# Kernel tuning notes

Measured on AMD Instinct MI355X. Metric: run time of the kernel, lower is better.

## Reference

```python
import jax, jax.numpy as jnp
import numpy as np
from jax import lax

B, C, IC, H, W = 4, 64, 32, 64, 64


def _conv(x, w, b, stride, pad):
    y = lax.conv_general_dilated(
        x, w, (stride, stride), [(pad, pad), (pad, pad)],
        dimension_numbers=('NCHW', 'OIHW', 'NCHW'))
    return y + b[None, :, None, None]


def setup_inputs() -> dict:
    key = jax.random.key(0)
    ks = jax.random.split(key, 15)
    s = 0.05
    inp = {
        'x': jax.random.normal(ks[0], (B, C, H, W), jnp.float32),
        # GEunit convs (3x3)
        'd1_w': jax.random.normal(ks[1], (C, C, 3, 3), jnp.float32) * s,
        'd1_b': jax.random.normal(ks[2], (C,), jnp.float32) * s,
        'd2_w': jax.random.normal(ks[3], (C, C, 3, 3), jnp.float32) * s,
        'd2_b': jax.random.normal(ks[4], (C,), jnp.float32) * s,
        'd3_w': jax.random.normal(ks[5], (C, C, 3, 3), jnp.float32) * s,
        'd3_b': jax.random.normal(ks[6], (C,), jnp.float32) * s,
        # 1x1 projections
        'g_w': jax.random.normal(ks[7], (IC, C, 1, 1), jnp.float32) * s,
        'g_b': jax.random.normal(ks[8], (IC,), jnp.float32) * s,
        'th_w': jax.random.normal(ks[9], (IC, C, 1, 1), jnp.float32) * s,
        'th_b': jax.random.normal(ks[10], (IC,), jnp.float32) * s,
        'ph_w': jax.random.normal(ks[11], (IC, C, 1, 1), jnp.float32) * s,
        'ph_b': jax.random.normal(ks[12], (IC,), jnp.float32) * s,
        # output projection (zero-init in original; random here for nontrivial baseline)
        'w_w': jax.random.normal(ks[13], (C, IC, 1, 1), jnp.float32) * s,
        'w_b': jax.random.normal(ks[14], (C,), jnp.float32) * s,
    }
    return inp


def _forward(x, d1_w, d1_b, d2_w, d2_b, d3_w, d3_b,
             g_w, g_b, th_w, th_b, ph_w, ph_b, w_w, w_b):
    lrelu = lambda v: jnp.where(v >= 0, v, 0.2 * v)
    y = lrelu(_conv(x, d1_w, d1_b, 2, 1))
    y = lrelu(_conv(y, d2_w, d2_b, 2, 1))
    y = _conv(y, d3_w, d3_b, 2, 1)
    y = jax.image.resize(y, (x.shape[0], x.shape[1], x.shape[2], x.shape[3]),
                         method='bilinear')  # align_corners=False equivalent
    am = jax.nn.sigmoid(y) * x  # attention_map, [B,C,H,W]

    b, c, h, w = am.shape
    n = h * w
    g_x = _conv(am, g_w, g_b, 1, 0).reshape(b, IC, n)      # [B,IC,N]
    theta = _conv(am, th_w, th_b, 1, 0).reshape(b, IC, n)  # [B,IC,N]
    phi = _conv(am, ph_w, ph_b, 1, 0).reshape(b, IC, n)    # [B,IC,N]

    # f[b,i,j] = theta[:, i] . phi[:, j];  softmax over dim=1 (the i axis)
    f = jnp.einsum('bci,bcj->bij', theta, phi)             # [B,N,N]
    f_div_C = jax.nn.softmax(f, axis=1)
    y2 = jnp.einsum('bij,bjc->bic', f_div_C, g_x.transpose(0, 2, 1))  # [B,N,IC]
    y2 = y2.transpose(0, 2, 1).reshape(b, IC, h, w)

    W_y = _conv(y2, w_w, w_b, 1, 0)
    z = W_y + am
    return z * x


def reference(x, d1_w, d1_b, d2_w, d2_b, d3_w, d3_b,
              g_w, g_b, th_w, th_b, ph_w, ph_b, w_w, w_b):
    return _forward(x, d1_w, d1_b, d2_w, d2_b, d3_w, d3_b,
                    g_w, g_b, th_w, th_b, ph_w, ph_b, w_w, w_b)
```

## Files before the change

kernel.cpp:

```cpp
#include <hip/hip_runtime.h>

#define B_ 4
#define C_ 64
#define IC_ 32
#define N_ 4096
#define LOG2E 1.44269504088896341f

typedef __attribute__((ext_vector_type(8))) short short8;
typedef __attribute__((ext_vector_type(4))) float floatx4;
typedef unsigned short ushort_t;

__device__ __forceinline__ unsigned short f2bf(float f) {
  unsigned u = __float_as_uint(f);
  u += 0x7FFFu + ((u >> 16) & 1u);
  return (unsigned short)(u >> 16);
}
__device__ __forceinline__ float bf2f(unsigned short h) {
  return __uint_as_float(((unsigned)h) << 16);
}

__global__ void __launch_bounds__(256) pack_xw_k(
    const float* __restrict__ x, unsigned short* __restrict__ xclp,
    const float* __restrict__ d1_w, const float* __restrict__ d2_w, const float* __restrict__ d3_w,
    const float* __restrict__ th_w, const float* __restrict__ ph_w, const float* __restrict__ g_w,
    const float* __restrict__ th_b, const float* __restrict__ ph_b, const float* __restrict__ g_b,
    unsigned short* __restrict__ wpk, unsigned short* __restrict__ wproj, float* __restrict__ bproj)
{
  __shared__ float s[64][65];
  const int t = threadIdx.x;
  if (blockIdx.x < 256) {
    const int b = blockIdx.x >> 6, h = blockIdx.x & 63;
    for (int idx = t; idx < 4096; idx += 256) {
      int c = idx >> 6, w = idx & 63;
      s[c][w] = x[((size_t)(b * 64 + c)) * 4096 + h * 64 + w];
    }
    __syncthreads();
    for (int idx = t; idx < 4096; idx += 256) {
      int w = idx >> 6, c = idx & 63;
      xclp[(((size_t)b * 66 + h + 1) * 66 + (w + 1)) * 64 + c] = f2bf(s[c][w]);
    }
  } else {
    const int tid = (blockIdx.x - 256) * 256 + t;
    for (int idx = tid; idx < 3 * 36864; idx += 16 * 256) {
      int cv = idx / 36864, r = idx % 36864;
      int tap = r / 4096, r2 = r % 4096;
      int oc = r2 >> 6, ic = r2 & 63;
      const float* src = (cv == 0) ? d1_w : (cv == 1) ? d2_w : d3_w;
      wpk[(size_t)cv * 36864 + tap * 4096 + oc * 64 + ic] = f2bf(src[oc * 576 + ic * 9 + tap]);
    }
    for (int idx = tid; idx < 6144; idx += 16 * 256) {
      int m = idx >> 6, ic = idx & 63;
      float v = (m < 32) ? LOG2E * th_w[m * 64 + ic]
              : (m < 64) ? ph_w[(m - 32) * 64 + ic]
                         : g_w[(m - 64) * 64 + ic];
      wproj[m * 64 + ic] = f2bf(v);
    }
    for (int m = tid; m < 96; m += 16 * 256) {
      bproj[m] = (m < 32) ? LOG2E * th_b[m] : (m < 64) ? ph_b[m - 32] : g_b[m - 64];
    }
  }
}

template<int IN_PW, int OUT_H, bool LRELU, bool OUT_BF16>
__global__ void __launch_bounds__(64) convmf_k(
    const unsigned short* __restrict__ xin, const unsigned short* __restrict__ wp,
    const float* __restrict__ bias, unsigned short* __restrict__ obf,
    float* __restrict__ of32)
{
  constexpr int NTILES = OUT_H * OUT_H / 16;
  const int lane = threadIdx.x;
  const int n15 = lane & 15, quad = lane >> 4;
  int bx = blockIdx.x;
  const int octile = bx & 3; bx >>= 2;
  const int otile = bx % NTILES;
  const int b = bx / NTILES;
  const int o = otile * 16 + n15;
  const int oh = o / OUT_H, ow = o % OUT_H;
  const unsigned short* xb = xin + (size_t)b * IN_PW * IN_PW * 64;
  floatx4 acc = {0.f, 0.f, 0.f, 0.f};
#pragma unroll
  for (int tap = 0; tap < 9; ++tap) {
    const int kh = tap / 3, kw = tap % 3;
    const unsigned short* xpix = xb + ((size_t)(oh * 2 + kh) * IN_PW + (ow * 2 + kw)) * 64;
#pragma unroll
    for (int ks = 0; ks < 2; ++ks) {
      short8 af = *reinterpret_cast<const short8*>(
          wp + ((size_t)tap * 64 + octile * 16 + n15) * 64 + ks * 32 + quad * 8);
      short8 bf = *reinterpret_cast<const short8*>(xpix + ks * 32 + quad * 8);
      acc = __builtin_amdgcn_mfma_f32_16x16x32_bf16(af, bf, acc, 0, 0, 0);
    }
  }
  const float4 bv = *reinterpret_cast<const float4*>(bias + octile * 16 + quad * 4);
  float v[4] = {acc[0] + bv.x, acc[1] + bv.y, acc[2] + bv.z, acc[3] + bv.w};
  if (LRELU) {
#pragma unroll
    for (int r = 0; r < 4; ++r) v[r] = (v[r] >= 0.f) ? v[r] : 0.2f * v[r];
  }
  if (OUT_BF16) {
    constexpr int OPW = OUT_H + 2;
    unsigned short pk[4];
#pragma unroll
    for (int r = 0; r < 4; ++r) pk[r] = f2bf(v[r]);
    *reinterpret_cast<uint2*>(
        obf + (((size_t)b * OPW + oh + 1) * OPW + (ow + 1)) * 64 + octile * 16 + quad * 4) =
        *reinterpret_cast<uint2*>(pk);
  } else {
    *reinterpret_cast<float4*>(
        of32 + ((size_t)b * OUT_H * OUT_H + o) * 64 + octile * 16 + quad * 4) =
        *reinterpret_cast<float4*>(v);
  }
}

__global__ void __launch_bounds__(256) upsproj_k(
    const unsigned short* __restrict__ y2clp, const unsigned short* __restrict__ wp3,
    const float* __restrict__ b3, const float* __restrict__ x,
    const unsigned short* __restrict__ wproj, const float* __restrict__ bproj,
    unsigned short* __restrict__ am_cl, unsigned short* __restrict__ thph,
    unsigned short* __restrict__ g16)
{
  const int b = blockIdx.x >> 6, oh = blockIdx.x & 63;
  const int t = threadIdx.x;
  __shared__ float s0[512], s1[512];
  __shared__ unsigned short s_am[64][72];
  float sh = (oh + 0.5f) * 0.125f - 0.5f;
  float fh = floorf(sh); float ah = sh - fh; int h0 = (int)fh;
  int h0c = min(7, max(0, h0)), h1c = min(7, max(0, h0 + 1));
  {
    const int wave = t >> 6, lane = t & 63;
    const int n15 = lane & 15, quad = lane >> 4;
    const int hrow = (n15 < 8) ? h0c : h1c;
    const int ow8 = n15 & 7;
    const unsigned short* xb2 = y2clp + (size_t)b * 18 * 18 * 64;
    floatx4 acc = {0.f, 0.f, 0.f, 0.f};
#pragma unroll
    for (int tap = 0; tap < 9; ++tap) {
      const int kh = tap / 3, kw = tap % 3;
      const unsigned short* xpix = xb2 + ((size_t)(hrow * 2 + kh) * 18 + (ow8 * 2 + kw)) * 64;
#pragma unroll
      for (int ks = 0; ks < 2; ++ks) {
        short8 af = *reinterpret_cast<const short8*>(
            wp3 + ((size_t)tap * 64 + wave * 16 + n15) * 64 + ks * 32 + quad * 8);
        short8 bf = *reinterpret_cast<const short8*>(xpix + ks * 32 + quad * 8);
        acc = __builtin_amdgcn_mfma_f32_16x16x32_bf16(af, bf, acc, 0, 0, 0);
      }
    }
    const float4 bv = *reinterpret_cast<const float4*>(b3 + wave * 16 + quad * 4);
    float4 st = {acc[0] + bv.x, acc[1] + bv.y, acc[2] + bv.z, acc[3] + bv.w};
    float* dst = (n15 < 8) ? s0 : s1;
    *reinterpret_cast<float4*>(&dst[(size_t)ow8 * 64 + wave * 16 + quad * 4]) = st;
  }
  __syncthreads();
  {
    const int ow = t >> 2, cq = t & 3;
    float sw = (ow + 0.5f) * 0.125f - 0.5f;
    float fw = floorf(sw); float aw = sw - fw; int w0 = (int)fw;
    int w0c = min(7, max(0, w0)), w1c = min(7, max(0, w0 + 1));
    const int n = oh * 64 + ow;
    const float* xb = x + (size_t)b * 64 * 4096 + n;
    unsigned short* ap = am_cl + ((size_t)b * N_ + n) * 64 + cq * 16;
#pragma unroll
    for (int u = 0; u < 4; ++u) {
      int c0 = cq * 16 + u * 4;
      float4 a00 = *reinterpret_cast<const float4*>(&s0[w0c * 64 + c0]);
      float4 a01 = *reinterpret_cast<const float4*>(&s0[w1c * 64 + c0]);
      float4 a10 = *reinterpret_cast<const float4*>(&s1[w0c * 64 + c0]);
      float4 a11 = *reinterpret_cast<const float4*>(&s1[w1c * 64 + c0]);
      float i0[4] = {a00.x * (1.f - aw) + a01.x * aw, a00.y * (1.f - aw) + a01.y * aw,
                     a00.z * (1.f - aw) + a01.z * aw, a00.w * (1.f - aw) + a01.w * aw};
      float i1[4] = {a10.x * (1.f - aw) + a11.x * aw, a10.y * (1.f - aw) + a11.y * aw,
                     a10.z * (1.f - aw) + a11.z * aw, a10.w * (1.f - aw) + a11.w * aw};
      unsigned short pk[4];
#pragma unroll
      for (int vi = 0; vi < 4; ++vi) {
        float vv = i0[vi] * (1.f - ah) + i1[vi] * ah;
        float xv = xb[(size_t)(c0 + vi) * 4096];
        float sig = 1.f / (1.f + __expf(-vv));
        pk[vi] = f2bf(sig * xv);
      }
      uint2 pkt = *reinterpret_cast<uint2*>(pk);
      *reinterpret_cast<uint2*>(ap + u * 4) = pkt;
      *reinterpret_cast<uint2*>(&s_am[ow][c0]) = pkt;
    }
  }
  __syncthreads();
  const int wave = t >> 6, lane = t & 63;
  const int n15 = lane & 15, quad = lane >> 4;
  const int n = oh * 64 + wave * 16 + n15;
  const unsigned short* srow = &s_am[wave * 16 + n15][0];
  const short8 bf0 = *reinterpret_cast<const short8*>(srow + quad * 8);
  const short8 bf1 = *reinterpret_cast<const short8*>(srow + 32 + quad * 8);
#pragma unroll
  for (int mt = 0; mt < 6; ++mt) {
    short8 a0 = *reinterpret_cast<const short8*>(wproj + ((size_t)mt * 16 + n15) * 64 + quad * 8);
    short8 a1 = *reinterpret_cast<const short8*>(wproj + ((size_t)mt * 16 + n15) * 64 + 32 + quad * 8);
    floatx4 acc = {0.f, 0.f, 0.f, 0.f};
    acc = __builtin_amdgcn_mfma_f32_16x16x32_bf16(a0, bf0, acc, 0, 0, 0);
    acc = __builtin_amdgcn_mfma_f32_16x16x32_bf16(a1, bf1, acc, 0, 0, 0);
    const float4 bv = *reinterpret_cast<const float4*>(bproj + mt * 16 + quad * 4);
    float v[4] = {acc[0] + bv.x, acc[1] + bv.y, acc[2] + bv.z, acc[3] + bv.w};
    if (mt < 4) {
      unsigned short pk[4];
#pragma unroll
      for (int r = 0; r < 4; ++r) pk[r] = f2bf(v[r]);
      *reinterpret_cast<uint2*>(thph + ((size_t)b * N_ + n) * 64 + mt * 16 + quad * 4) =
          *reinterpret_cast<uint2*>(pk);
    } else {
#pragma unroll
      for (int r = 0; r < 4; ++r)
        g16[((size_t)b * 32 + (mt - 4) * 16 + quad * 4 + r) * N_ + n] = f2bf(v[r]);
    }
  }
}

__global__ void __launch_bounds__(256) attn_stats_k(
    const unsigned short* __restrict__ thph, float* __restrict__ lpart)
{
  const int b  = blockIdx.y;
  const int iz = blockIdx.z;
  const int t = threadIdx.x, wave = t >> 6, lane = t & 63;
  const int n15 = lane & 15, quad = lane >> 4;
  const int jw = blockIdx.x * 256 + wave * 64;
  const unsigned short* base = thph + (size_t)b * N_ * 64;
  short8 bv[4];
#pragma unroll
  for (int v = 0; v < 4; ++v)
    bv[v] = *reinterpret_cast<const short8*>(base + (size_t)(jw + v * 16 + n15) * 64 + 32 + quad * 8);
  float ls[4] = {0.f, 0.f, 0.f, 0.f};
  const unsigned short* ap = base + (size_t)(iz * 256 + n15) * 64 + quad * 8;
  short8 ac = *reinterpret_cast<const short8*>(ap);
  for (int st = 0; st < 16; ++st) {
    short8 an = *reinterpret_cast<const short8*>(ap + (size_t)((st < 15) ? st + 1 : st) * 1024);
#pragma unroll
    for (int v = 0; v < 4; ++v) {
      floatx4 z = {0.f, 0.f, 0.f, 0.f};
      z = __builtin_amdgcn_mfma_f32_16x16x32_bf16(ac, bv[v], z, 0, 0, 0);
      ls[v] += (__builtin_amdgcn_exp2f(z[0]) + __builtin_amdgcn_exp2f(z[1]))
             + (__builtin_amdgcn_exp2f(z[2]) + __builtin_amdgcn_exp2f(z[3]));
    }
    ac = an;
  }
#pragma unroll
  for (int v = 0; v < 4; ++v) {
    ls[v] += __shfl_xor(ls[v], 16);
    ls[v] += __shfl_xor(ls[v], 32);
  }
  if (quad == 0) {
#pragma unroll
    for (int v = 0; v < 4; ++v)
      lpart[((size_t)iz * B_ + b) * N_ + jw + v * 16 + n15] = ls[v];
  }
}

__global__ void __launch_bounds__(256) scale_g_k(
    const float* __restrict__ lpart, unsigned short* __restrict__ g16)
{
  const int b = blockIdx.y;
  const int c0 = blockIdx.z * 8;
  const int j = blockIdx.x * 256 + threadIdx.x;
  float l = 0.f;
#pragma unroll
  for (int iz = 0; iz < 16; ++iz) l += lpart[((size_t)iz * B_ + b) * N_ + j];
  const float rl = 1.f / l;
  unsigned short* gp = g16 + ((size_t)b * 32 + c0) * N_ + j;
#pragma unroll
  for (int c = 0; c < 8; ++c) {
    gp[(size_t)c * N_] = f2bf(bf2f(gp[(size_t)c * N_]) * rl);
  }
}

#define PHI_PITCH 40
#define G_PITCH   136
__global__ void __launch_bounds__(256, 2) attn_pv_k(
    const unsigned short* __restrict__ thph, const unsigned short* __restrict__ g16,
    unsigned short* __restrict__ y2p)
{
  const int b  = blockIdx.y;
  const int jq = blockIdx.z;
  const int t = threadIdx.x, wave = t >> 6, lane = t & 63;
  const int n15 = lane & 15, quad = lane >> 4;
  const int iw = blockIdx.x * 128 + wave * 32;
  const unsigned short* base = thph + (size_t)b * N_ * 64;
  const unsigned short* gs   = g16  + (size_t)b * 32 * N_;
  __shared__ unsigned short phi_lds[2][128 * PHI_PITCH];
  __shared__ unsigned short g_lds[2][32 * G_PITCH];

  const short8 bth0 = *reinterpret_cast<const short8*>(base + (size_t)(iw + n15) * 64 + quad * 8);
  const short8 bth1 = *reinterpret_cast<const short8*>(base + (size_t)(iw + 16 + n15) * 64 + quad * 8);
  floatx4 Y00 = {0.f, 0.f, 0.f, 0.f}, Y01 = {0.f, 0.f, 0.f, 0.f};
  floatx4 Y10 = {0.f, 0.f, 0.f, 0.f}, Y11 = {0.f, 0.f, 0.f, 0.f};

  const int rphi = wave * 32 + (lane >> 2), cph = lane & 3;
  const int cg   = wave * 8  + (lane >> 4), chg = lane & 15;

  uint4 sp0, sp1, sg0, sg1;
  const int jbase = jq * 1024;
  sp0 = *reinterpret_cast<const uint4*>(base + (size_t)(jbase + rphi) * 64 + 32 + cph * 8);
  sp1 = *reinterpret_cast<const uint4*>(base + (size_t)(jbase + rphi + 16) * 64 + 32 + cph * 8);
  sg0 = *reinterpret_cast<const uint4*>(gs + (size_t)cg * N_ + jbase + chg * 8);
  sg1 = *reinterpret_cast<const uint4*>(gs + (size_t)(cg + 4) * N_ + jbase + chg * 8);
  *reinterpret_cast<uint4*>(&phi_lds[0][rphi * PHI_PITCH + cph * 8]) = sp0;
  *reinterpret_cast<uint4*>(&phi_lds[0][(rphi + 16) * PHI_PITCH + cph * 8]) = sp1;
  *reinterpret_cast<uint4*>(&g_lds[0][cg * G_PITCH + chg * 8]) = sg0;
  *reinterpret_cast<uint4*>(&g_lds[0][(cg + 4) * G_PITCH + chg * 8]) = sg1;
  __syncthreads();

  int j0 = jbase;
  for (int ch = 0; ch < 8; ++ch, j0 += 128) {
    const int cur = ch & 1;
    if (ch < 7) {
      const int jn = j0 + 128;
      sp0 = *reinterpret_cast<const uint4*>(base + (size_t)(jn + rphi) * 64 + 32 + cph * 8);
      sp1 = *reinterpret_cast<const uint4*>(base + (size_t)(jn + rphi + 16) * 64 + 32 + cph * 8);
      sg0 = *reinterpret_cast<const uint4*>(gs + (size_t)cg * N_ + jn + chg * 8);
      sg1 = *reinterpret_cast<const uint4*>(gs + (size_t)(cg + 4) * N_ + jn + chg * 8);
    }
    const unsigned short* phb = &phi_lds[cur][0];
    const unsigned short* glb = &g_lds[cur][0];
#pragma unroll
    for (int sg = 0; sg < 4; ++sg) {
      unsigned pk0[4], pk1[4];
#pragma unroll
      for (int jtl = 0; jtl < 2; ++jtl) {
        const int jt = sg * 2 + jtl;
        short8 aph = *reinterpret_cast<const short8*>(phb + (jt * 16 + n15) * PHI_PITCH + quad * 8);
        floatx4 z0 = {0.f, 0.f, 0.f, 0.f}, z1 = {0.f, 0.f, 0.f, 0.f};
        z0 = __builtin_amdgcn_mfma_f32_16x16x32_bf16(aph, bth0, z0, 0, 0, 0);
        z1 = __builtin_amdgcn_mfma_f32_16x16x32_bf16(aph, bth1, z1, 0, 0, 0);
        float a0 = __builtin_amdgcn_exp2f(z0[0]), a1 = __builtin_amdgcn_exp2f(z0[1]);
        float a2 = __builtin_amdgcn_exp2f(z0[2]), a3 = __builtin_amdgcn_exp2f(z0[3]);
        float b0f = __builtin_amdgcn_exp2f(z1[0]), b1f = __builtin_amdgcn_exp2f(z1[1]);
        float b2f = __builtin_amdgcn_exp2f(z1[2]), b3f = __builtin_amdgcn_exp2f(z1[3]);
        pk0[jtl * 2 + 0] = __builtin_amdgcn_perm(__float_as_uint(a1), __float_as_uint(a0), 0x07060302);
        pk0[jtl * 2 + 1] = __builtin_amdgcn_perm(__float_as_uint(a3), __float_as_uint(a2), 0x07060302);
        pk1[jtl * 2 + 0] = __builtin_amdgcn_perm(__float_as_uint(b1f), __float_as_uint(b0f), 0x07060302);
        pk1[jtl * 2 + 1] = __builtin_amdgcn_perm(__float_as_uint(b3f), __float_as_uint(b2f), 0x07060302);
      }
      union { unsigned u[4]; short8 v; } pa0, pa1, gb0, gb1;
      pa0.u[0] = pk0[0]; pa0.u[1] = pk0[1]; pa0.u[2] = pk0[2]; pa0.u[3] = pk0[3];
      pa1.u[0] = pk1[0]; pa1.u[1] = pk1[1]; pa1.u[2] = pk1[2]; pa1.u[3] = pk1[3];
      const unsigned short* gr0 = glb + n15 * G_PITCH + sg * 32 + quad * 4;
      const unsigned short* gr1 = glb + (16 + n15) * G_PITCH + sg * 32 + quad * 4;
      uint2 lo0 = *reinterpret_cast<const uint2*>(gr0);
      uint2 hi0 = *reinterpret_cast<const uint2*>(gr0 + 16);
      uint2 lo1 = *reinterpret_cast<const uint2*>(gr1);
      uint2 hi1 = *reinterpret_cast<const uint2*>(gr1 + 16);
      gb0.u[0] = lo0.x; gb0.u[1] = lo0.y; gb0.u[2] = hi0.x; gb0.u[3] = hi0.y;
      gb1.u[0] = lo1.x; gb1.u[1] = lo1.y; gb1.u[2] = hi1.x; gb1.u[3] = hi1.y;
      Y00 = __builtin_amdgcn_mfma_f32_16x16x32_bf16(pa0.v, gb0.v, Y00, 0, 0, 0);
      Y01 = __builtin_amdgcn_mfma_f32_16x16x32_bf16(pa0.v, gb1.v, Y01, 0, 0, 0);
      Y10 = __builtin_amdgcn_mfma_f32_16x16x32_bf16(pa1.v, gb0.v, Y10, 0, 0, 0);
      Y11 = __builtin_amdgcn_mfma_f32_16x16x32_bf16(pa1.v, gb1.v, Y11, 0, 0, 0);
    }
    if (ch < 7) {
      const int nb = cur ^ 1;
      *reinterpret_cast<uint4*>(&phi_lds[nb][rphi * PHI_PITCH + cph * 8]) = sp0;
      *reinterpret_cast<uint4*>(&phi_lds[nb][(rphi + 16) * PHI_PITCH + cph * 8]) = sp1;
      *reinterpret_cast<uint4*>(&g_lds[nb][cg * G_PITCH + chg * 8]) = sg0;
      *reinterpret_cast<uint4*>(&g_lds[nb][(cg + 4) * G_PITCH + chg * 8]) = sg1;
    }
    __syncthreads();
  }
  unsigned w00[2], w01[2], w10[2], w11[2];
  w00[0] = ((unsigned)f2bf(Y00[1]) << 16) | f2bf(Y00[0]);
  w00[1] = ((unsigned)f2bf(Y00[3]) << 16) | f2bf(Y00[2]);
  w01[0] = ((unsigned)f2bf(Y01[1]) << 16) | f2bf(Y01[0]);
  w01[1] = ((unsigned)f2bf(Y01[3]) << 16) | f2bf(Y01[2]);
  w10[0] = ((unsigned)f2bf(Y10[1]) << 16) | f2bf(Y10[0]);
  w10[1] = ((unsigned)f2bf(Y10[3]) << 16) | f2bf(Y10[2]);
  w11[0] = ((unsigned)f2bf(Y11[1]) << 16) | f2bf(Y11[0]);
  w11[1] = ((unsigned)f2bf(Y11[3]) << 16) | f2bf(Y11[2]);
  const size_t orow = ((size_t)jq * B_ + b) * 32;
  *reinterpret_cast<uint2*>(y2p + (orow + n15) * N_ + iw + quad * 4) =
      *reinterpret_cast<uint2*>(w00);
  *reinterpret_cast<uint2*>(y2p + (orow + 16 + n15) * N_ + iw + quad * 4) =
      *reinterpret_cast<uint2*>(w01);
  *reinterpret_cast<uint2*>(y2p + (orow + n15) * N_ + iw + 16 + quad * 4) =
      *reinterpret_cast<uint2*>(w10);
  *reinterpret_cast<uint2*>(y2p + (orow + 16 + n15) * N_ + iw + 16 + quad * 4) =
      *reinterpret_cast<uint2*>(w11);
}

__global__ void __launch_bounds__(256) final_k(
    const unsigned short* __restrict__ y2p, const float* __restrict__ w_w,
    const float* __restrict__ w_b, const unsigned short* __restrict__ am_cl,
    const float* __restrict__ x, float* __restrict__ out)
{
  const int n0 = (blockIdx.x * 256 + threadIdx.x) * 2;
  const int o0 = blockIdx.y * 8;
  const int b  = blockIdx.z;
  float a0[8], a1[8];
#pragma unroll
  for (int u = 0; u < 8; ++u) { a0[u] = w_b[o0 + u]; a1[u] = a0[u]; }
  for (int c = 0; c < 32; ++c) {
    float s0 = 0.f, s1 = 0.f;
#pragma unroll
    for (int ph = 0; ph < 4; ++ph) {
      unsigned v = *reinterpret_cast<const unsigned*>(
          y2p + (((size_t)ph * B_ + b) * 32 + c) * N_ + n0);
      s0 += bf2f((unsigned short)(v & 0xffffu));
      s1 += bf2f((unsigned short)(v >> 16));
    }
#pragma unroll
    for (int u = 0; u < 8; ++u) {
      float wv = w_w[(o0 + u) * 32 + c];
      a0[u] += wv * s0; a1[u] += wv * s1;
    }
  }
  const short8 am0 = *reinterpret_cast<const short8*>(am_cl + ((size_t)b * N_ + n0) * 64 + o0);
  const short8 am1 = *reinterpret_cast<const short8*>(am_cl + ((size_t)b * N_ + n0 + 1) * 64 + o0);
#pragma unroll
  for (int u = 0; u < 8; ++u) {
    size_t off = ((size_t)b * 64 + o0 + u) * N_ + n0;
    float2 xv = *reinterpret_cast<const float2*>(x + off);
    float2 ov;
    ov.x = (a0[u] + bf2f((unsigned short)am0[u])) * xv.x;
    ov.y = (a1[u] + bf2f((unsigned short)am1[u])) * xv.y;
    *reinterpret_cast<float2*>(out + off) = ov;
  }
}

extern "C" void kernel_launch(void* const* d_in, const int* in_sizes, int n_in,
                              void* d_out, int out_size, void* d_ws, size_t ws_size,
                              hipStream_t stream) {
  const float* x    = (const float*)d_in[0];
  const float* d1_w = (const float*)d_in[1];
  const float* d1_b = (const float*)d_in[2];
  const float* d2_w = (const float*)d_in[3];
  const float* d2_b = (const float*)d_in[4];
  const float* d3_w = (const float*)d_in[5];
  const float* d3_b = (const float*)d_in[6];
  const float* g_w  = (const float*)d_in[7];
  const float* g_b  = (const float*)d_in[8];
  const float* th_w = (const float*)d_in[9];
  const float* th_b = (const float*)d_in[10];
  const float* ph_w = (const float*)d_in[11];
  const float* ph_b = (const float*)d_in[12];
  const float* w_w  = (const float*)d_in[13];
  const float* w_b  = (const float*)d_in[14];
  float* out = (float*)d_out;

  char* p = (char*)d_ws;
  unsigned short* am_cl = (unsigned short*)p;  p += (size_t)B_ * N_ * 64 * 2;
  unsigned short* thph  = (unsigned short*)p;  p += (size_t)B_ * N_ * 64 * 2;
  unsigned short* g16   = (unsigned short*)p;  p += (size_t)B_ * 32 * N_ * 2;
  float* lpart          = (float*)p;           p += (size_t)16 * B_ * N_ * 4;
  unsigned short* y2p   = (unsigned short*)p;  p += (size_t)4 * B_ * 32 * N_ * 2;
  unsigned short* wpk   = (unsigned short*)p;  p += (size_t)3 * 36864 * 2;
  unsigned short* wproj = (unsigned short*)p;  p += (size_t)96 * 64 * 2;
  float* bproj          = (float*)p;           p += (size_t)96 * 4;
  char* zbase = p;
  unsigned short* xclp  = (unsigned short*)p;  p += (size_t)B_ * 66 * 66 * 64 * 2;
  unsigned short* y1clp = (unsigned short*)p;  p += (size_t)B_ * 34 * 34 * 64 * 2;
  unsigned short* y2clp = (unsigned short*)p;  p += (size_t)B_ * 18 * 18 * 64 * 2;
  const size_t zbytes = (size_t)(p - zbase);

  hipMemsetAsync(zbase, 0, zbytes, stream);
  pack_xw_k<<<272, 256, 0, stream>>>(x, xclp, d1_w, d2_w, d3_w, th_w, ph_w, g_w,
                                     th_b, ph_b, g_b, wpk, wproj, bproj);
  convmf_k<66, 32, true,  true ><<<1024, 64, 0, stream>>>(xclp,  wpk,         d1_b, y1clp, nullptr);
  convmf_k<34, 16, true,  true ><<<256,  64, 0, stream>>>(y1clp, wpk + 36864, d2_b, y2clp, nullptr);
  upsproj_k<<<256, 256, 0, stream>>>(y2clp, wpk + 2 * 36864, d3_b, x, wproj, bproj,
                                     am_cl, thph, g16);
  attn_stats_k<<<dim3(16, 4, 16), 256, 0, stream>>>(thph, lpart);
  scale_g_k<<<dim3(16, 4, 4), 256, 0, stream>>>(lpart, g16);
  attn_pv_k<<<dim3(32, 4, 4), 256, 0, stream>>>(thph, g16, y2p);
  final_k<<<dim3(8, 8, 4), 256, 0, stream>>>(y2p, w_w, w_b, am_cl, x, out);
}
```

Before: 151.6 us.

## Fuse all stages into one cooperative persistent kernel with grid syncs

Replaces the memset plus eight separate launches with a single cooperative kernel of 256 blocks. Phases are separated by grid.sync, and a multi-kernel fallback is kept in case the cooperative launch fails. Padding zeroing moves into the pack phase, and the scale_g pass is folded into the PV phase by computing reciprocal row sums in shared memory. The stats and PV work is reshaped so each wave or block handles larger tiles. This removes launch and inter-kernel gaps, but each phase is now limited to 256 blocks at one block per CU, and grid syncs add their own cost.

```diff
diff --git a/kernel.cpp b/kernel.cpp
--- a/kernel.cpp
+++ b/kernel.cpp
@@ -1,4 +1,7 @@
 #include <hip/hip_runtime.h>
+#include <hip/hip_cooperative_groups.h>
+
+namespace cg = cooperative_groups;
 
 #define B_ 4
 #define C_ 64
@@ -8,7 +11,6 @@
 
 typedef __attribute__((ext_vector_type(8))) short short8;
 typedef __attribute__((ext_vector_type(4))) float floatx4;
-typedef unsigned short ushort_t;
 
 __device__ __forceinline__ unsigned short f2bf(float f) {
   unsigned u = __float_as_uint(f);
@@ -19,58 +21,75 @@
   return __uint_as_float(((unsigned)h) << 16);
 }
 
-__global__ void __launch_bounds__(256) pack_xw_k(
-    const float* __restrict__ x, unsigned short* __restrict__ xclp,
-    const float* __restrict__ d1_w, const float* __restrict__ d2_w, const float* __restrict__ d3_w,
-    const float* __restrict__ th_w, const float* __restrict__ ph_w, const float* __restrict__ g_w,
-    const float* __restrict__ th_b, const float* __restrict__ ph_b, const float* __restrict__ g_b,
-    unsigned short* __restrict__ wpk, unsigned short* __restrict__ wproj, float* __restrict__ bproj)
-{
-  __shared__ float s[64][65];
-  const int t = threadIdx.x;
-  if (blockIdx.x < 256) {
-    const int b = blockIdx.x >> 6, h = blockIdx.x & 63;
+struct Params {
+  const float* x;
+  const float* d1_w; const float* d1_b;
+  const float* d2_w; const float* d2_b;
+  const float* d3_w; const float* d3_b;
+  const float* g_w;  const float* g_b;
+  const float* th_w; const float* th_b;
+  const float* ph_w; const float* ph_b;
+  const float* w_w;  const float* w_b;
+  float* out;
+  unsigned short* am_cl; unsigned short* thph; unsigned short* g16;
+  float* lpart; unsigned short* y2p;
+  unsigned short* wpk; unsigned short* wproj; float* bproj;
+  unsigned short* xclp; unsigned short* y1clp; unsigned short* y2clp;
+};
+
+#define SMEM_BYTES 42496
+
+__device__ __forceinline__ void phase_pack(const Params& p, char* smem) {
+  const int bid = blockIdx.x, t = threadIdx.x;
+  {
+    float (*s)[65] = reinterpret_cast<float(*)[65]>(smem);
+    const int b = bid >> 6, h = bid & 63;
     for (int idx = t; idx < 4096; idx += 256) {
       int c = idx >> 6, w = idx & 63;
-      s[c][w] = x[((size_t)(b * 64 + c)) * 4096 + h * 64 + w];
+      s[c][w] = p.x[((size_t)(b * 64 + c)) * 4096 + h * 64 + w];
     }
     __syncthreads();
     for (int idx = t; idx < 4096; idx += 256) {
       int w = idx >> 6, c = idx & 63;
-      xclp[(((size_t)b * 66 + h + 1) * 66 + (w + 1)) * 64 + c] = f2bf(s[c][w]);
-    }
-  } else {
-    const int tid = (blockIdx.x - 256) * 256 + t;
-    for (int idx = tid; idx < 3 * 36864; idx += 16 * 256) {
-      int cv = idx / 36864, r = idx % 36864;
-      int tap = r / 4096, r2 = r % 4096;
-      int oc = r2 >> 6, ic = r2 & 63;
-      const float* src = (cv == 0) ? d1_w : (cv == 1) ? d2_w : d3_w;
-      wpk[(size_t)cv * 36864 + tap * 4096 + oc * 64 + ic] = f2bf(src[oc * 576 + ic * 9 + tap]);
-    }
-    for (int idx = tid; idx < 6144; idx += 16 * 256) {
-      int m = idx >> 6, ic = idx & 63;
-      float v = (m < 32) ? LOG2E * th_w[m * 64 + ic]
-              : (m < 64) ? ph_w[(m - 32) * 64 + ic]
-                         : g_w[(m - 64) * 64 + ic];
-      wproj[m * 64 + ic] = f2bf(v);
-    }
-    for (int m = tid; m < 96; m += 16 * 256) {
-      bproj[m] = (m < 32) ? LOG2E * th_b[m] : (m < 64) ? ph_b[m - 32] : g_b[m - 64];
-    }
-  }
-}
-
-template<int IN_PW, int OUT_H, bool LRELU, bool OUT_BF16>
-__global__ void __launch_bounds__(64) convmf_k(
-    const unsigned short* __restrict__ xin, const unsigned short* __restrict__ wp,
-    const float* __restrict__ bias, unsigned short* __restrict__ obf,
-    float* __restrict__ of32)
-{
+      p.xclp[(((size_t)b * 66 + h + 1) * 66 + (w + 1)) * 64 + c] = f2bf(s[c][w]);
+    }
+  }
+  const int gt = bid * 256 + t;
+  for (int idx = gt; idx < 3 * 36864; idx += 65536) {
+    int cv = idx / 36864, r = idx % 36864;
+    int tap = r / 4096, r2 = r % 4096;
+    int oc = r2 >> 6, ic = r2 & 63;
+    const float* src = (cv == 0) ? p.d1_w : (cv == 1) ? p.d2_w : p.d3_w;
+    p.wpk[(size_t)cv * 36864 + tap * 4096 + oc * 64 + ic] = f2bf(src[oc * 576 + ic * 9 + tap]);
+  }
+  if (gt < 6144) {
+    int m = gt >> 6, ic = gt & 63;
+    float v = (m < 32) ? LOG2E * p.th_w[m * 64 + ic]
+            : (m < 64) ? p.ph_w[(m - 32) * 64 + ic]
+                       : p.g_w[(m - 64) * 64 + ic];
+    p.wproj[m * 64 + ic] = f2bf(v);
+  }
+  if (gt < 96)
+    p.bproj[gt] = (gt < 32) ? LOG2E * p.th_b[gt] : (gt < 64) ? p.ph_b[gt - 32] : p.g_b[gt - 64];
+  uint4 z4 = {0u, 0u, 0u, 0u};
+  if (gt < 4 * 66 * 66) {
+    int r = gt % 4356, h = r / 66, w = r % 66;
+    if (h == 0 || h == 65 || w == 0 || w == 65) {
+      uint4* d = reinterpret_cast<uint4*>(p.xclp + (size_t)gt * 64);
+#pragma unroll
+      for (int q = 0; q < 8; ++q) d[q] = z4;
+    }
+  }
+  if (gt < 36992) reinterpret_cast<uint4*>(p.y1clp)[gt] = z4;
+  if (gt < 10368) reinterpret_cast<uint4*>(p.y2clp)[gt] = z4;
+}
+
+template<int IN_PW, int OUT_H>
+__device__ __forceinline__ void phase_conv(const unsigned short* xin, const unsigned short* wp,
+                                           const float* bias, unsigned short* obf, int wid, int lane) {
   constexpr int NTILES = OUT_H * OUT_H / 16;
-  const int lane = threadIdx.x;
   const int n15 = lane & 15, quad = lane >> 4;
-  int bx = blockIdx.x;
+  int bx = wid;
   const int octile = bx & 3; bx >>= 2;
   const int otile = bx % NTILES;
   const int b = bx / NTILES;
@@ -92,36 +111,24 @@
   }
   const float4 bv = *reinterpret_cast<const float4*>(bias + octile * 16 + quad * 4);
   float v[4] = {acc[0] + bv.x, acc[1] + bv.y, acc[2] + bv.z, acc[3] + bv.w};
-  if (LRELU) {
-#pragma unroll
-    for (int r = 0; r < 4; ++r) v[r] = (v[r] >= 0.f) ? v[r] : 0.2f * v[r];
-  }
-  if (OUT_BF16) {
-    constexpr int OPW = OUT_H + 2;
-    unsigned short pk[4];
-#pragma unroll
-    for (int r = 0; r < 4; ++r) pk[r] = f2bf(v[r]);
-    *reinterpret_cast<uint2*>(
-        obf + (((size_t)b * OPW + oh + 1) * OPW + (ow + 1)) * 64 + octile * 16 + quad * 4) =
-        *reinterpret_cast<uint2*>(pk);
-  } else {
-    *reinterpret_cast<float4*>(
-        of32 + ((size_t)b * OUT_H * OUT_H + o) * 64 + octile * 16 + quad * 4) =
-        *reinterpret_cast<float4*>(v);
-  }
-}
-
-__global__ void __launch_bounds__(256) upsproj_k(
-    const unsigned short* __restrict__ y2clp, const unsigned short* __restrict__ wp3,
-    const float* __restrict__ b3, const float* __restrict__ x,
-    const unsigned short* __restrict__ wproj, const float* __restrict__ bproj,
-    unsigned short* __restrict__ am_cl, unsigned short* __restrict__ thph,
-    unsigned short* __restrict__ g16)
-{
-  const int b = blockIdx.x >> 6, oh = blockIdx.x & 63;
-  const int t = threadIdx.x;
-  __shared__ float s0[512], s1[512];
-  __shared__ unsigned short s_am[64][72];
+#pragma unroll
+  for (int r = 0; r < 4; ++r) v[r] = (v[r] >= 0.f) ? v[r] : 0.2f * v[r];
+  constexpr int OPW = OUT_H + 2;
+  unsigned short pk[4];
+#pragma unroll
+  for (int r = 0; r < 4; ++r) pk[r] = f2bf(v[r]);
+  *reinterpret_cast<uint2*>(
+      obf + (((size_t)b * OPW + oh + 1) * OPW + (ow + 1)) * 64 + octile * 16 + quad * 4) =
+      *reinterpret_cast<uint2*>(pk);
+}
+
+__device__ __forceinline__ void phase_upsproj(const Params& p, char* smem) {
+  const int bid = blockIdx.x, t = threadIdx.x;
+  const int b = bid >> 6, oh = bid & 63;
+  float* s0 = reinterpret_cast<float*>(smem);
+  float* s1 = s0 + 512;
+  unsigned short* s_am = reinterpret_cast<unsigned short*>(smem + 4096);
+  const unsigned short* wp3 = p.wpk + 2 * 36864;
   float sh = (oh + 0.5f) * 0.125f - 0.5f;
   float fh = floorf(sh); float ah = sh - fh; int h0 = (int)fh;
   int h0c = min(7, max(0, h0)), h1c = min(7, max(0, h0 + 1));
@@ -130,7 +137,7 @@
     const int n15 = lane & 15, quad = lane >> 4;
     const int hrow = (n15 < 8) ? h0c : h1c;
     const int ow8 = n15 & 7;
-    const unsigned short* xb2 = y2clp + (size_t)b * 18 * 18 * 64;
+    const unsigned short* xb2 = p.y2clp + (size_t)b * 18 * 18 * 64;
     floatx4 acc = {0.f, 0.f, 0.f, 0.f};
 #pragma unroll
     for (int tap = 0; tap < 9; ++tap) {
@@ -144,7 +151,7 @@
         acc = __builtin_amdgcn_mfma_f32_16x16x32_bf16(af, bf, acc, 0, 0, 0);
       }
     }
-    const float4 bv = *reinterpret_cast<const float4*>(b3 + wave * 16 + quad * 4);
+    const float4 bv = *reinterpret_cast<const float4*>(p.d3_b + wave * 16 + quad * 4);
     float4 st = {acc[0] + bv.x, acc[1] + bv.y, acc[2] + bv.z, acc[3] + bv.w};
     float* dst = (n15 < 8) ? s0 : s1;
     *reinterpret_cast<float4*>(&dst[(size_t)ow8 * 64 + wave * 16 + quad * 4]) = st;
@@ -156,8 +163,8 @@
     float fw = floorf(sw); float aw = sw - fw; int w0 = (int)fw;
     int w0c = min(7, max(0, w0)), w1c = min(7, max(0, w0 + 1));
     const int n = oh * 64 + ow;
-    const float* xb = x + (size_t)b * 64 * 4096 + n;
-    unsigned short* ap = am_cl + ((size_t)b * N_ + n) * 64 + cq * 16;
+    const float* xb = p.x + (size_t)b * 64 * 4096 + n;
+    unsigned short* ap = p.am_cl + ((size_t)b * N_ + n) * 64 + cq * 16;
 #pragma unroll
     for (int u = 0; u < 4; ++u) {
       int c0 = cq * 16 + u * 4;
@@ -179,59 +186,57 @@
       }
       uint2 pkt = *reinterpret_cast<uint2*>(pk);
       *reinterpret_cast<uint2*>(ap + u * 4) = pkt;
-      *reinterpret_cast<uint2*>(&s_am[ow][c0]) = pkt;
+      *reinterpret_cast<uint2*>(&s_am[ow * 72 + c0]) = pkt;
     }
   }
   __syncthreads();
   const int wave = t >> 6, lane = t & 63;
   const int n15 = lane & 15, quad = lane >> 4;
   const int n = oh * 64 + wave * 16 + n15;
-  const unsigned short* srow = &s_am[wave * 16 + n15][0];
+  const unsigned short* srow = &s_am[(wave * 16 + n15) * 72];
   const short8 bf0 = *reinterpret_cast<const short8*>(srow + quad * 8);
   const short8 bf1 = *reinterpret_cast<const short8*>(srow + 32 + quad * 8);
 #pragma unroll
   for (int mt = 0; mt < 6; ++mt) {
-    short8 a0 = *reinterpret_cast<const short8*>(wproj + ((size_t)mt * 16 + n15) * 64 + quad * 8);
-    short8 a1 = *reinterpret_cast<const short8*>(wproj + ((size_t)mt * 16 + n15) * 64 + 32 + quad * 8);
+    short8 a0 = *reinterpret_cast<const short8*>(p.wproj + ((size_t)mt * 16 + n15) * 64 + quad * 8);
+    short8 a1 = *reinterpret_cast<const short8*>(p.wproj + ((size_t)mt * 16 + n15) * 64 + 32 + quad * 8);
     floatx4 acc = {0.f, 0.f, 0.f, 0.f};
     acc = __builtin_amdgcn_mfma_f32_16x16x32_bf16(a0, bf0, acc, 0, 0, 0);
     acc = __builtin_amdgcn_mfma_f32_16x16x32_bf16(a1, bf1, acc, 0, 0, 0);
-    const float4 bv = *reinterpret_cast<const float4*>(bproj + mt * 16 + quad * 4);
+    const float4 bv = *reinterpret_cast<const float4*>(p.bproj + mt * 16 + quad * 4);
     float v[4] = {acc[0] + bv.x, acc[1] + bv.y, acc[2] + bv.z, acc[3] + bv.w};
     if (mt < 4) {
       unsigned short pk[4];
 #pragma unroll
       for (int r = 0; r < 4; ++r) pk[r] = f2bf(v[r]);
-      *reinterpret_cast<uint2*>(thph + ((size_t)b * N_ + n) * 64 + mt * 16 + quad * 4) =
+      *reinterpret_cast<uint2*>(p.thph + ((size_t)b * N_ + n) * 64 + mt * 16 + quad * 4) =
           *reinterpret_cast<uint2*>(pk);
     } else {
 #pragma unroll
       for (int r = 0; r < 4; ++r)
-        g16[((size_t)b * 32 + (mt - 4) * 16 + quad * 4 + r) * N_ + n] = f2bf(v[r]);
-    }
-  }
-}
-
-__global__ void __launch_bounds__(256) attn_stats_k(
-    const unsigned short* __restrict__ thph, float* __restrict__ lpart)
-{
-  const int b  = blockIdx.y;
-  const int iz = blockIdx.z;
-  const int t = threadIdx.x, wave = t >> 6, lane = t & 63;
+        p.g16[((size_t)b * 32 + (mt - 4) * 16 + quad * 4 + r) * N_ + n] = f2bf(v[r]);
+    }
+  }
+}
+
+__device__ __forceinline__ void phase_stats(const Params& p, int wid, int lane) {
   const int n15 = lane & 15, quad = lane >> 4;
-  const int jw = blockIdx.x * 256 + wave * 64;
-  const unsigned short* base = thph + (size_t)b * N_ * 64;
-  short8 bv[4];
-#pragma unroll
-  for (int v = 0; v < 4; ++v)
-    bv[v] = *reinterpret_cast<const short8*>(base + (size_t)(jw + v * 16 + n15) * 64 + 32 + quad * 8);
-  float ls[4] = {0.f, 0.f, 0.f, 0.f};
+  const int iz = wid >> 6, b = (wid >> 4) & 3, jc = wid & 15;
+  const int j0 = jc * 256;
+  const unsigned short* base = p.thph + (size_t)b * N_ * 64;
+  short8 bv[16];
+#pragma unroll
+  for (int v = 0; v < 16; ++v)
+    bv[v] = *reinterpret_cast<const short8*>(base + (size_t)(j0 + v * 16 + n15) * 64 + 32 + quad * 8);
+  float ls[16];
+#pragma unroll
+  for (int v = 0; v < 16; ++v) ls[v] = 0.f;
   const unsigned short* ap = base + (size_t)(iz * 256 + n15) * 64 + quad * 8;
   short8 ac = *reinterpret_cast<const short8*>(ap);
   for (int st = 0; st < 16; ++st) {
     short8 an = *reinterpret_cast<const short8*>(ap + (size_t)((st < 15) ? st + 1 : st) * 1024);
 #pragma unroll
-    for (int v = 0; v < 4; ++v) {
+    for (int v = 0; v < 16; ++v) {
       floatx4 z = {0.f, 0.f, 0.f, 0.f};
       z = __builtin_amdgcn_mfma_f32_16x16x32_bf16(ac, bv[v], z, 0, 0, 0);
       ls[v] += (__builtin_amdgcn_exp2f(z[0]) + __builtin_amdgcn_exp2f(z[1]))
@@ -240,70 +245,55 @@
     ac = an;
   }
 #pragma unroll
-  for (int v = 0; v < 4; ++v) {
+  for (int v = 0; v < 16; ++v) {
     ls[v] += __shfl_xor(ls[v], 16);
     ls[v] += __shfl_xor(ls[v], 32);
   }
   if (quad == 0) {
 #pragma unroll
-    for (int v = 0; v < 4; ++v)
-      lpart[((size_t)iz * B_ + b) * N_ + jw + v * 16 + n15] = ls[v];
-  }
-}
-
-__global__ void __launch_bounds__(256) scale_g_k(
-    const float* __restrict__ lpart, unsigned short* __restrict__ g16)
-{
-  const int b = blockIdx.y;
-  const int c0 = blockIdx.z * 8;
-  const int j = blockIdx.x * 256 + threadIdx.x;
-  float l = 0.f;
-#pragma unroll
-  for (int iz = 0; iz < 16; ++iz) l += lpart[((size_t)iz * B_ + b) * N_ + j];
-  const float rl = 1.f / l;
-  unsigned short* gp = g16 + ((size_t)b * 32 + c0) * N_ + j;
-#pragma unroll
-  for (int c = 0; c < 8; ++c) {
-    gp[(size_t)c * N_] = f2bf(bf2f(gp[(size_t)c * N_]) * rl);
+    for (int v = 0; v < 16; ++v)
+      p.lpart[((size_t)iz * B_ + b) * N_ + j0 + v * 16 + n15] = ls[v];
   }
 }
 
 #define PHI_PITCH 40
 #define G_PITCH   136
-__global__ void __launch_bounds__(256, 2) attn_pv_k(
-    const unsigned short* __restrict__ thph, const unsigned short* __restrict__ g16,
-    unsigned short* __restrict__ y2p)
-{
-  const int b  = blockIdx.y;
-  const int jq = blockIdx.z;
-  const int t = threadIdx.x, wave = t >> 6, lane = t & 63;
+__device__ __forceinline__ void phase_pv(const Params& p, char* smem) {
+  const int bid = blockIdx.x, t = threadIdx.x;
+  const int wave = t >> 6, lane = t & 63;
   const int n15 = lane & 15, quad = lane >> 4;
-  const int iw = blockIdx.x * 128 + wave * 32;
-  const unsigned short* base = thph + (size_t)b * N_ * 64;
-  const unsigned short* gs   = g16  + (size_t)b * 32 * N_;
-  __shared__ unsigned short phi_lds[2][128 * PHI_PITCH];
-  __shared__ unsigned short g_lds[2][32 * G_PITCH];
-
-  const short8 bth0 = *reinterpret_cast<const short8*>(base + (size_t)(iw + n15) * 64 + quad * 8);
-  const short8 bth1 = *reinterpret_cast<const short8*>(base + (size_t)(iw + 16 + n15) * 64 + quad * 8);
-  floatx4 Y00 = {0.f, 0.f, 0.f, 0.f}, Y01 = {0.f, 0.f, 0.f, 0.f};
-  floatx4 Y10 = {0.f, 0.f, 0.f, 0.f}, Y11 = {0.f, 0.f, 0.f, 0.f};
-
+  const int ixp = bid & 15, b = (bid >> 4) & 3, jq = bid >> 6;
+  unsigned short* phi_lds = reinterpret_cast<unsigned short*>(smem);
+  unsigned short* g_lds   = reinterpret_cast<unsigned short*>(smem + 20480);
+  float* rl_lds           = reinterpret_cast<float*>(smem + 37888);
+  const unsigned short* base = p.thph + (size_t)b * N_ * 64;
+  const unsigned short* gs   = p.g16  + (size_t)b * 32 * N_;
+  const int jbase = jq * 1024;
+  for (int jj = t; jj < 1024; jj += 256) {
+    float l = 0.f;
+#pragma unroll
+    for (int iz = 0; iz < 16; ++iz) l += p.lpart[((size_t)iz * B_ + b) * N_ + jbase + jj];
+    rl_lds[jj] = 1.f / l;
+  }
+  const int iw = ixp * 256 + wave * 32;
+  const short8 bthA0 = *reinterpret_cast<const short8*>(base + (size_t)(iw + n15) * 64 + quad * 8);
+  const short8 bthA1 = *reinterpret_cast<const short8*>(base + (size_t)(iw + 16 + n15) * 64 + quad * 8);
+  const short8 bthB0 = *reinterpret_cast<const short8*>(base + (size_t)(iw + 128 + n15) * 64 + quad * 8);
+  const short8 bthB1 = *reinterpret_cast<const short8*>(base + (size_t)(iw + 144 + n15) * 64 + quad * 8);
+  floatx4 YA00 = {0,0,0,0}, YA01 = {0,0,0,0}, YA10 = {0,0,0,0}, YA11 = {0,0,0,0};
+  floatx4 YB00 = {0,0,0,0}, YB01 = {0,0,0,0}, YB10 = {0,0,0,0}, YB11 = {0,0,0,0};
   const int rphi = wave * 32 + (lane >> 2), cph = lane & 3;
-  const int cg   = wave * 8  + (lane >> 4), chg = lane & 15;
-
+  const int cg_  = wave * 8  + (lane >> 4), chg = lane & 15;
   uint4 sp0, sp1, sg0, sg1;
-  const int jbase = jq * 1024;
   sp0 = *reinterpret_cast<const uint4*>(base + (size_t)(jbase + rphi) * 64 + 32 + cph * 8);
   sp1 = *reinterpret_cast<const uint4*>(base + (size_t)(jbase + rphi + 16) * 64 + 32 + cph * 8);
-  sg0 = *reinterpret_cast<const uint4*>(gs + (size_t)cg * N_ + jbase + chg * 8);
-  sg1 = *reinterpret_cast<const uint4*>(gs + (size_t)(cg + 4) * N_ + jbase + chg * 8);
-  *reinterpret_cast<uint4*>(&phi_lds[0][rphi * PHI_PITCH + cph * 8]) = sp0;
-  *reinterpret_cast<uint4*>(&phi_lds[0][(rphi + 16) * PHI_PITCH + cph * 8]) = sp1;
-  *reinterpret_cast<uint4*>(&g_lds[0][cg * G_PITCH + chg * 8]) = sg0;
-  *reinterpret_cast<uint4*>(&g_lds[0][(cg + 4) * G_PITCH + chg * 8]) = sg1;
+  sg0 = *reinterpret_cast<const uint4*>(gs + (size_t)cg_ * N_ + jbase + chg * 8);
+  sg1 = *reinterpret_cast<const uint4*>(gs + (size_t)(cg_ + 4) * N_ + jbase + chg * 8);
+  *reinterpret_cast<uint4*>(&phi_lds[rphi * PHI_PITCH + cph * 8]) = sp0;
+  *reinterpret_cast<uint4*>(&phi_lds[(rphi + 16) * PHI_PITCH + cph * 8]) = sp1;
+  *reinterpret_cast<uint4*>(&g_lds[cg_ * G_PITCH + chg * 8]) = sg0;
+  *reinterpret_cast<uint4*>(&g_lds[(cg_ + 4) * G_PITCH + chg * 8]) = sg1;
   __syncthreads();
-
   int j0 = jbase;
   for (int ch = 0; ch < 8; ++ch, j0 += 128) {
     const int cur = ch & 1;
@@ -311,158 +301,211 @@
       const int jn = j0 + 128;
       sp0 = *reinterpret_cast<const uint4*>(base + (size_t)(jn + rphi) * 64 + 32 + cph * 8);
       sp1 = *reinterpret_cast<const uint4*>(base + (size_t)(jn + rphi + 16) * 64 + 32 + cph * 8);
-      sg0 = *reinterpret_cast<const uint4*>(gs + (size_t)cg * N_ + jn + chg * 8);
-      sg1 = *reinterpret_cast<const uint4*>(gs + (size_t)(cg + 4) * N_ + jn + chg * 8);
-    }
-    const unsigned short* phb = &phi_lds[cur][0];
-    const unsigned short* glb = &g_lds[cur][0];
-#pragma unroll
-    for (int sg = 0; sg < 4; ++sg) {
-      unsigned pk0[4], pk1[4];
+      sg0 = *reinterpret_cast<const uint4*>(gs + (size_t)cg_ * N_ + jn + chg * 8);
+      sg1 = *reinterpret_cast<const uint4*>(gs + (size_t)(cg_ + 4) * N_ + jn + chg * 8);
+    }
+    const unsigned short* phb = phi_lds + cur * (128 * PHI_PITCH);
+    const unsigned short* glb = g_lds + cur * (32 * G_PITCH);
+#pragma unroll
+    for (int sg_ = 0; sg_ < 4; ++sg_) {
+      unsigned pkA0[4], pkA1[4], pkB0[4], pkB1[4];
 #pragma unroll
       for (int jtl = 0; jtl < 2; ++jtl) {
-        const int jt = sg * 2 + jtl;
+        const int jt = sg_ * 2 + jtl;
         short8 aph = *reinterpret_cast<const short8*>(phb + (jt * 16 + n15) * PHI_PITCH + quad * 8);
-        floatx4 z0 = {0.f, 0.f, 0.f, 0.f}, z1 = {0.f, 0.f, 0.f, 0.f};
-        z0 = __builtin_amdgcn_mfma_f32_16x16x32_bf16(aph, bth0, z0, 0, 0, 0);
-        z1 = __builtin_amdgcn_mfma_f32_16x16x32_bf16(aph, bth1, z1, 0, 0, 0);
-        float a0 = __builtin_amdgcn_exp2f(z0[0]), a1 = __builtin_amdgcn_exp2f(z0[1]);
-        float a2 = __builtin_amdgcn_exp2f(z0[2]), a3 = __builtin_amdgcn_exp2f(z0[3]);
-        float b0f = __builtin_amdgcn_exp2f(z1[0]), b1f = __builtin_amdgcn_exp2f(z1[1]);
-        float b2f = __builtin_amdgcn_exp2f(z1[2]), b3f = __builtin_amdgcn_exp2f(z1[3]);
-        pk0[jtl * 2 + 0] = __builtin_amdgcn_perm(__float_as_uint(a1), __float_as_uint(a0), 0x07060302);
-        pk0[jtl * 2 + 1] = __builtin_amdgcn_perm(__float_as_uint(a3), __float_as_uint(a2), 0x07060302);
-        pk1[jtl * 2 + 0] = __builtin_amdgcn_perm(__float_as_uint(b1f), __float_as_uint(b0f), 0x07060302);
-        pk1[jtl * 2 + 1] = __builtin_amdgcn_perm(__float_as_uint(b3f), __float_as_uint(b2f), 0x07060302);
+        float4 rlv = *reinterpret_cast<const float4*>(&rl_lds[ch * 128 + jt * 16 + quad * 4]);
+        floatx4 zA0 = {0,0,0,0}, zA1 = {0,0,0,0}, zB0 = {0,0,0,0}, zB1 = {0,0,0,0};
+        zA0 = __builtin_amdgcn_mfma_f32_16x16x32_bf16(aph, bthA0, zA0, 0, 0, 0);
+        zA1 = __builtin_amdgcn_mfma_f32_16x16x32_bf16(aph, bthA1, zA1, 0, 0, 0);
+        zB0 = __builtin_amdgcn_mfma_f32_16x16x32_bf16(aph, bthB0, zB0, 0, 0, 0);
+        zB1 = __builtin_amdgcn_mfma_f32_16x16x32_bf16(aph, bthB1, zB1, 0, 0, 0);
+#define PK_(Z, PK)                                                                  \
+        {                                                                           \
+          float e0 = __builtin_amdgcn_exp2f(Z[0]) * rlv.x;                          \
+          float e1 = __builtin_amdgcn_exp2f(Z[1]) * rlv.y;                          \
+          float e2 = __builtin_amdgcn_exp2f(Z[2]) * rlv.z;                          \
+          float e3 = __builtin_amdgcn_exp2f(Z[3]) * rlv.w;                          \
+          PK[jtl * 2 + 0] = __builtin_amdgcn_perm(__float_as_uint(e1), __float_as_uint(e0), 0x07060302); \
+          PK[jtl * 2 + 1] = __builtin_amdgcn_perm(__float_as_uint(e3), __float_as_uint(e2), 0x07060302); \
+        }
+        PK_(zA0, pkA0) PK_(zA1, pkA1) PK_(zB0, pkB0) PK_(zB1, pkB1)
+#undef PK_
       }
-      union { unsigned u[4]; short8 v; } pa0, pa1, gb0, gb1;
-      pa0.u[0] = pk0[0]; pa0.u[1] = pk0[1]; pa0.u[2] = pk0[2]; pa0.u[3] = pk0[3];
-      pa1.u[0] = pk1[0]; pa1.u[1] = pk1[1]; pa1.u[2] = pk1[2]; pa1.u[3] = pk1[3];
-      const unsigned short* gr0 = glb + n15 * G_PITCH + sg * 32 + quad * 4;
-      const unsigned short* gr1 = glb + (16 + n15) * G_PITCH + sg * 32 + quad * 4;
+      union U8 { unsigned u[4]; short8 v; };
+      U8 paA0, paA1, paB0, paB1, gb0, gb1;
+#pragma unroll
+      for (int q = 0; q < 4; ++q) {
+        paA0.u[q] = pkA0[q]; paA1.u[q] = pkA1[q];
+        paB0.u[q] = pkB0[q]; paB1.u[q] = pkB1[q];
+      }
+      const unsigned short* gr0 = glb + n15 * G_PITCH + sg_ * 32 + quad * 4;
+      const unsigned short* gr1 = glb + (16 + n15) * G_PITCH + sg_ * 32 + quad * 4;
       uint2 lo0 = *reinterpret_cast<const uint2*>(gr0);
       uint2 hi0 = *reinterpret_cast<const uint2*>(gr0 + 16);
       uint2 lo1 = *reinterpret_cast<const uint2*>(gr1);
       uint2 hi1 = *reinterpret_cast<const uint2*>(gr1 + 16);
       gb0.u[0] = lo0.x; gb0.u[1] = lo0.y; gb0.u[2] = hi0.x; gb0.u[3] = hi0.y;
       gb1.u[0] = lo1.x; gb1.u[1] = lo1.y; gb1.u[2] = hi1.x; gb1.u[3] = hi1.y;
-      Y00 = __builtin_amdgcn_mfma_f32_16x16x32_bf16(pa0.v, gb0.v, Y00, 0, 0, 0);
-      Y01 = __builtin_amdgcn_mfma_f32_16x16x32_bf16(pa0.v, gb1.v, Y01, 0, 0, 0);
-      Y10 = __builtin_amdgcn_mfma_f32_16x16x32_bf16(pa1.v, gb0.v, Y10, 0, 0, 0);
-      Y11 = __builtin_amdgcn_mfma_f32_16x16x32_bf16(pa1.v, gb1.v, Y11, 0, 0, 0);
+      YA00 = __builtin_amdgcn_mfma_f32_16x16x32_bf16(paA0.v, gb0.v, YA00, 0, 0, 0);
+      YA01 = __builtin_amdgcn_mfma_f32_16x16x32_bf16(paA0.v, gb1.v, YA01, 0, 0, 0);
+      YA10 = __builtin_amdgcn_mfma_f32_16x16x32_bf16(paA1.v, gb0.v, YA10, 0, 0, 0);
+      YA11 = __builtin_amdgcn_mfma_f32_16x16x32_bf16(paA1.v, gb1.v, YA11, 0, 0, 0);
+      YB00 = __builtin_amdgcn_mfma_f32_16x16x32_bf16(paB0.v, gb0.v, YB00, 0, 0, 0);
+      YB01 = __builtin_amdgcn_mfma_f32_16x16x32_bf16(paB0.v, gb1.v, YB01, 0, 0, 0);
+      YB10 = __builtin_amdgcn_mfma_f32_16x16x32_bf16(paB1.v, gb0.v, YB10, 0, 0, 0);
+      YB11 = __builtin_amdgcn_mfma_f32_16x16x32_bf16(paB1.v, gb1.v, YB11, 0, 0, 0);
     }
     if (ch < 7) {
       const int nb = cur ^ 1;
-      *reinterpret_cast<uint4*>(&phi_lds[nb][rphi * PHI_PITCH + cph * 8]) = sp0;
-      *reinterpret_cast<uint4*>(&phi_lds[nb][(rphi + 16) * PHI_PITCH + cph * 8]) = sp1;
-      *reinterpret_cast<uint4*>(&g_lds[nb][cg * G_PITCH + chg * 8]) = sg0;
-      *reinterpret_cast<uint4*>(&g_lds[nb][(cg + 4) * G_PITCH + chg * 8]) = sg1;
+      *reinterpret_cast<uint4*>(&phi_lds[nb * (128 * PHI_PITCH) + rphi * PHI_PITCH + cph * 8]) = sp0;
+      *reinterpret_cast<uint4*>(&phi_lds[nb * (128 * PHI_PITCH) + (rphi + 16) * PHI_PITCH + cph * 8]) = sp1;
+      *reinterpret_cast<uint4*>(&g_lds[nb * (32 * G_PITCH) + cg_ * G_PITCH + chg * 8]) = sg0;
+      *reinterpret_cast<uint4*>(&g_lds[nb * (32 * G_PITCH) + (cg_ + 4) * G_PITCH + chg * 8]) = sg1;
     }
     __syncthreads();
   }
-  unsigned w00[2], w01[2], w10[2], w11[2];
-  w00[0] = ((unsigned)f2bf(Y00[1]) << 16) | f2bf(Y00[0]);
-  w00[1] = ((unsigned)f2bf(Y00[3]) << 16) | f2bf(Y00[2]);
-  w01[0] = ((unsigned)f2bf(Y01[1]) << 16) | f2bf(Y01[0]);
-  w01[1] = ((unsigned)f2bf(Y01[3]) << 16) | f2bf(Y01[2]);
-  w10[0] = ((unsigned)f2bf(Y10[1]) << 16) | f2bf(Y10[0]);
-  w10[1] = ((unsigned)f2bf(Y10[3]) << 16) | f2bf(Y10[2]);
-  w11[0] = ((unsigned)f2bf(Y11[1]) << 16) | f2bf(Y11[0]);
-  w11[1] = ((unsigned)f2bf(Y11[3]) << 16) | f2bf(Y11[2]);
   const size_t orow = ((size_t)jq * B_ + b) * 32;
-  *reinterpret_cast<uint2*>(y2p + (orow + n15) * N_ + iw + quad * 4) =
-      *reinterpret_cast<uint2*>(w00);
-  *reinterpret_cast<uint2*>(y2p + (orow + 16 + n15) * N_ + iw + quad * 4) =
-      *reinterpret_cast<uint2*>(w01);
-  *reinterpret_cast<uint2*>(y2p + (orow + n15) * N_ + iw + 16 + quad * 4) =
-      *reinterpret_cast<uint2*>(w10);
-  *reinterpret_cast<uint2*>(y2p + (orow + 16 + n15) * N_ + iw + 16 + quad * 4) =
-      *reinterpret_cast<uint2*>(w11);
-}
-
-__global__ void __launch_bounds__(256) final_k(
-    const unsigned short* __restrict__ y2p, const float* __restrict__ w_w,
-    const float* __restrict__ w_b, const unsigned short* __restrict__ am_cl,
-    const float* __restrict__ x, float* __restrict__ out)
-{
-  const int n0 = (blockIdx.x * 256 + threadIdx.x) * 2;
-  const int o0 = blockIdx.y * 8;
-  const int b  = blockIdx.z;
+#define STY_(Y, ROW, COL)                                                            \
+  {                                                                                  \
+    unsigned w_[2];                                                                  \
+    w_[0] = ((unsigned)f2bf(Y[1]) << 16) | f2bf(Y[0]);                               \
+    w_[1] = ((unsigned)f2bf(Y[3]) << 16) | f2bf(Y[2]);                               \
+    *reinterpret_cast<uint2*>(p.y2p + (size_t)(ROW) * N_ + (COL) + quad * 4) =       \
+        *reinterpret_cast<uint2*>(w_);                                               \
+  }
+  STY_(YA00, orow + n15,      iw)
+  STY_(YA01, orow + 16 + n15, iw)
+  STY_(YA10, orow + n15,      iw + 16)
+  STY_(YA11, orow + 16 + n15, iw + 16)
+  STY_(YB00, orow + n15,      iw + 128)
+  STY_(YB01, orow + 16 + n15, iw + 128)
+  STY_(YB10, orow + n15,      iw + 144)
+  STY_(YB11, orow + 16 + n15, iw + 144)
+#undef STY_
+}
+
+__device__ __forceinline__ void phase_final(const Params& p) {
+  const int bid = blockIdx.x;
+  const int xb_ = bid & 7, ob = (bid >> 3) & 7, b = bid >> 6;
+  const int n0 = (xb_ * 256 + (int)threadIdx.x) * 2;
+  const int o0 = ob * 8;
   float a0[8], a1[8];
 #pragma unroll
-  for (int u = 0; u < 8; ++u) { a0[u] = w_b[o0 + u]; a1[u] = a0[u]; }
+  for (int u = 0; u < 8; ++u) { a0[u] = p.w_b[o0 + u]; a1[u] = a0[u]; }
   for (int c = 0; c < 32; ++c) {
     float s0 = 0.f, s1 = 0.f;
 #pragma unroll
     for (int ph = 0; ph < 4; ++ph) {
       unsigned v = *reinterpret_cast<const unsigned*>(
-          y2p + (((size_t)ph * B_ + b) * 32 + c) * N_ + n0);
+          p.y2p + (((size_t)ph * B_ + b) * 32 + c) * N_ + n0);
       s0 += bf2f((unsigned short)(v & 0xffffu));
       s1 += bf2f((unsigned short)(v >> 16));
     }
 #pragma unroll
     for (int u = 0; u < 8; ++u) {
-      float wv = w_w[(o0 + u) * 32 + c];
+      float wv = p.w_w[(o0 + u) * 32 + c];
       a0[u] += wv * s0; a1[u] += wv * s1;
     }
   }
-  const short8 am0 = *reinterpret_cast<const short8*>(am_cl + ((size_t)b * N_ + n0) * 64 + o0);
-  const short8 am1 = *reinterpret_cast<const short8*>(am_cl + ((size_t)b * N_ + n0 + 1) * 64 + o0);
+  const short8 am0 = *reinterpret_cast<const short8*>(p.am_cl + ((size_t)b * N_ + n0) * 64 + o0);
+  const short8 am1 = *reinterpret_cast<const short8*>(p.am_cl + ((size_t)b * N_ + n0 + 1) * 64 + o0);
 #pragma unroll
   for (int u = 0; u < 8; ++u) {
     size_t off = ((size_t)b * 64 + o0 + u) * N_ + n0;
-    float2 xv = *reinterpret_cast<const float2*>(x + off);
+    float2 xv = *reinterpret_cast<const float2*>(p.x + off);
     float2 ov;
     ov.x = (a0[u] + bf2f((unsigned short)am0[u])) * xv.x;
     ov.y = (a1[u] + bf2f((unsigned short)am1[u])) * xv.y;
-    *reinterpret_cast<float2*>(out + off) = ov;
-  }
+    *reinterpret_cast<float2*>(p.out + off) = ov;
+  }
+}
+
+__global__ void __launch_bounds__(256, 1) mega_k(Params p) {
+  __shared__ __align__(16) char smem[SMEM_BYTES];
+  cg::grid_group grid = cg::this_grid();
+  const int bid = blockIdx.x, t = threadIdx.x;
+  const int wave = t >> 6, lane = t & 63;
+  phase_pack(p, smem);
+  grid.sync();
+  phase_conv<66, 32>(p.xclp, p.wpk, p.d1_b, p.y1clp, bid * 4 + wave, lane);
+  grid.sync();
+  { int wid = bid * 4 + wave;
+    if (wid < 256) phase_conv<34, 16>(p.y1clp, p.wpk + 36864, p.d2_b, p.y2clp, wid, lane); }
+  grid.sync();
+  phase_upsproj(p, smem);
+  grid.sync();
+  phase_stats(p, bid * 4 + wave, lane);
+  grid.sync();
+  phase_pv(p, smem);
+  grid.sync();
+  phase_final(p);
+}
+
+__global__ void __launch_bounds__(256) ph0_k(Params p) {
+  __shared__ __align__(16) char smem[SMEM_BYTES];
+  phase_pack(p, smem);
+}
+__global__ void __launch_bounds__(256) ph1_k(Params p) {
+  phase_conv<66, 32>(p.xclp, p.wpk, p.d1_b, p.y1clp,
+                     blockIdx.x * 4 + (threadIdx.x >> 6), threadIdx.x & 63);
+}
+__global__ void __launch_bounds__(256) ph2_k(Params p) {
+  int wid = blockIdx.x * 4 + (threadIdx.x >> 6);
+  if (wid < 256) phase_conv<34, 16>(p.y1clp, p.wpk + 36864, p.d2_b, p.y2clp, wid, threadIdx.x & 63);
+}
+__global__ void __launch_bounds__(256) ph3_k(Params p) {
+  __shared__ __align__(16) char smem[SMEM_BYTES];
+  phase_upsproj(p, smem);
+}
+__global__ void __launch_bounds__(256) ph4_k(Params p) {
+  phase_stats(p, blockIdx.x * 4 + (threadIdx.x >> 6), threadIdx.x & 63);
+}
+__global__ void __launch_bounds__(256) ph5_k(Params p) {
+  __shared__ __align__(16) char smem[SMEM_BYTES];
+  phase_pv(p, smem);
+}
+__global__ void __launch_bounds__(256) ph6_k(Params p) {
+  phase_final(p);
 }
 
 extern "C" void kernel_launch(void* const* d_in, const int* in_sizes, int n_in,
                               void* d_out, int out_size, void* d_ws, size_t ws_size,
                               hipStream_t stream) {
-  const float* x    = (const float*)d_in[0];
-  const float* d1_w = (const float*)d_in[1];
-  const float* d1_b = (const float*)d_in[2];
-  const float* d2_w = (const float*)d_in[3];
-  const float* d2_b = (const float*)d_in[4];
-  const float* d3_w = (const float*)d_in[5];
-  const float* d3_b = (const float*)d_in[6];
-  const float* g_w  = (const float*)d_in[7];
-  const float* g_b  = (const float*)d_in[8];
-  const float* th_w = (const float*)d_in[9];
-  const float* th_b = (const float*)d_in[10];
-  const float* ph_w = (const float*)d_in[11];
-  const float* ph_b = (const float*)d_in[12];
-  const float* w_w  = (const float*)d_in[13];
-  const float* w_b  = (const float*)d_in[14];
-  float* out = (float*)d_out;
+  Params prm;
+  prm.x    = (const float*)d_in[0];
+  prm.d1_w = (const float*)d_in[1];  prm.d1_b = (const float*)d_in[2];
+  prm.d2_w = (const float*)d_in[3];  prm.d2_b = (const float*)d_in[4];
+  prm.d3_w = (const float*)d_in[5];  prm.d3_b = (const float*)d_in[6];
+  prm.g_w  = (const float*)d_in[7];  prm.g_b  = (const float*)d_in[8];
+  prm.th_w = (const float*)d_in[9];  prm.th_b = (const float*)d_in[10];
+  prm.ph_w = (const float*)d_in[11]; prm.ph_b = (const float*)d_in[12];
+  prm.w_w  = (const float*)d_in[13]; prm.w_b  = (const float*)d_in[14];
+  prm.out  = (float*)d_out;
 
   char* p = (char*)d_ws;
-  unsigned short* am_cl = (unsigned short*)p;  p += (size_t)B_ * N_ * 64 * 2;
-  unsigned short* thph  = (unsigned short*)p;  p += (size_t)B_ * N_ * 64 * 2;
-  unsigned short* g16   = (unsigned short*)p;  p += (size_t)B_ * 32 * N_ * 2;
-  float* lpart          = (float*)p;           p += (size_t)16 * B_ * N_ * 4;
-  unsigned short* y2p   = (unsigned short*)p;  p += (size_t)4 * B_ * 32 * N_ * 2;
-  unsigned short* wpk   = (unsigned short*)p;  p += (size_t)3 * 36864 * 2;
-  unsigned short* wproj = (unsigned short*)p;  p += (size_t)96 * 64 * 2;
-  float* bproj          = (float*)p;           p += (size_t)96 * 4;
-  char* zbase = p;
-  unsigned short* xclp  = (unsigned short*)p;  p += (size_t)B_ * 66 * 66 * 64 * 2;
-  unsigned short* y1clp = (unsigned short*)p;  p += (size_t)B_ * 34 * 34 * 64 * 2;
-  unsigned short* y2clp = (unsigned short*)p;  p += (size_t)B_ * 18 * 18 * 64 * 2;
-  const size_t zbytes = (size_t)(p - zbase);
-
-  hipMemsetAsync(zbase, 0, zbytes, stream);
-  pack_xw_k<<<272, 256, 0, stream>>>(x, xclp, d1_w, d2_w, d3_w, th_w, ph_w, g_w,
-                                     th_b, ph_b, g_b, wpk, wproj, bproj);
-  convmf_k<66, 32, true,  true ><<<1024, 64, 0, stream>>>(xclp,  wpk,         d1_b, y1clp, nullptr);
-  convmf_k<34, 16, true,  true ><<<256,  64, 0, stream>>>(y1clp, wpk + 36864, d2_b, y2clp, nullptr);
-  upsproj_k<<<256, 256, 0, stream>>>(y2clp, wpk + 2 * 36864, d3_b, x, wproj, bproj,
-                                     am_cl, thph, g16);
-  attn_stats_k<<<dim3(16, 4, 16), 256, 0, stream>>>(thph, lpart);
-  scale_g_k<<<dim3(16, 4, 4), 256, 0, stream>>>(lpart, g16);
-  attn_pv_k<<<dim3(32, 4, 4), 256, 0, stream>>>(thph, g16, y2p);
-  final_k<<<dim3(8, 8, 4), 256, 0, stream>>>(y2p, w_w, w_b, am_cl, x, out);
-}
+  prm.am_cl = (unsigned short*)p;  p += (size_t)B_ * N_ * 64 * 2;
+  prm.thph  = (unsigned short*)p;  p += (size_t)B_ * N_ * 64 * 2;
+  prm.g16   = (unsigned short*)p;  p += (size_t)B_ * 32 * N_ * 2;
+  prm.lpart = (float*)p;           p += (size_t)16 * B_ * N_ * 4;
+  prm.y2p   = (unsigned short*)p;  p += (size_t)4 * B_ * 32 * N_ * 2;
+  prm.wpk   = (unsigned short*)p;  p += (size_t)3 * 36864 * 2;
+  prm.wproj = (unsigned short*)p;  p += (size_t)96 * 64 * 2;
+  prm.bproj = (float*)p;           p += (size_t)96 * 4;
+  prm.xclp  = (unsigned short*)p;  p += (size_t)B_ * 66 * 66 * 64 * 2;
+  prm.y1clp = (unsigned short*)p;  p += (size_t)B_ * 34 * 34 * 64 * 2;
+  prm.y2clp = (unsigned short*)p;  p += (size_t)B_ * 18 * 18 * 64 * 2;
+
+  void* args[] = { (void*)&prm };
+  hipError_t err = hipLaunchCooperativeKernel((const void*)mega_k, dim3(256), dim3(256),
+                                              args, 0, stream);
+  if (err != hipSuccess) {
+    (void)hipGetLastError();
+    hipLaunchKernelGGL(ph0_k, dim3(256), dim3(256), 0, stream, prm);
+    hipLaunchKernelGGL(ph1_k, dim3(256), dim3(256), 0, stream, prm);
+    hipLaunchKernelGGL(ph2_k, dim3(256), dim3(256), 0, stream, prm);
+    hipLaunchKernelGGL(ph3_k, dim3(256), dim3(256), 0, stream, prm);
+    hipLaunchKernelGGL(ph4_k, dim3(256), dim3(256), 0, stream, prm);
+    hipLaunchKernelGGL(ph5_k, dim3(256), dim3(256), 0, stream, prm);
+    hipLaunchKernelGGL(ph6_k, dim3(256), dim3(256), 0, stream, prm);
+  }
+}
```

After: 362.1 us. 2.39x slower.
